# Optimization experiments

Measured on AMD Instinct MI355X. Metric: run time of the kernel, lower is better.

## Reference

```python
import jax, jax.numpy as jnp
import numpy as np

N = 50000   # nodes
IN = 256    # in_feats
OUT = 256   # out_feats
R = 4       # num relations
E = 80000   # edges per relation


def setup_inputs() -> dict:
    key = jax.random.key(0)
    ks = jax.random.split(key, 5)
    x = jax.random.normal(ks[0], (N, IN), jnp.float32)
    src = jax.random.randint(ks[1], (R, E), 0, N, jnp.int32)
    dst = jax.random.randint(ks[2], (R, E), 0, N, jnp.int32)
    # xavier_uniform with relu gain sqrt(2)
    limit = np.sqrt(2.0) * np.sqrt(6.0 / (IN + OUT))
    weight = jax.random.uniform(ks[3], (R, IN, OUT), jnp.float32, -limit, limit)
    self_loop_weight = jax.random.uniform(ks[4], (IN, OUT), jnp.float32, -limit, limit)
    bias = jnp.zeros((OUT,), jnp.float32)
    return dict(x=x, src=src, dst=dst, weight=weight,
                self_loop_weight=self_loop_weight, bias=bias)


def reference(x, src, dst, weight, self_loop_weight, bias):
    n = x.shape[0]

    def per_rel(s, d, W):
        # GraphConv(norm='right', weight=W): sum incoming messages, divide by
        # in-degree (clamped to 1), then matmul (in_feats == out_feats path).
        agg = jax.ops.segment_sum(x[s], d, num_segments=n)            # [N, IN]
        deg = jax.ops.segment_sum(jnp.ones(d.shape, x.dtype), d, num_segments=n)
        agg = agg / jnp.maximum(deg, 1.0)[:, None]
        return agg @ W                                                # [N, OUT]

    # HeteroGraphConv default aggregation: sum over relations
    msg = jax.vmap(per_rel)(src, dst, weight).sum(axis=0)             # [N, OUT]
    out = msg + x @ self_loop_weight + bias
    return jax.nn.relu(out)
```

## Files before the change

### kernel.cpp

```cpp
#include <hip/hip_runtime.h>

#define NODES 50000
#define FEAT  256
#define RELS  4
#define EDGES 80000
#define NEDGE (RELS * EDGES)
#define NB    (RELS * NODES)
#define NBSC  196

typedef __bf16 bf16x8  __attribute__((ext_vector_type(8)));
typedef float  floatx4 __attribute__((ext_vector_type(4)));

struct BF8U { union { unsigned short u[8]; bf16x8 v; uint4 q; }; };

static __device__ __forceinline__ unsigned short f2bf(float f) {
  union { float f; unsigned u; } v; v.f = f;
  unsigned r = v.u + 0x7FFFu + ((v.u >> 16) & 1u);
  return (unsigned short)(r >> 16);
}
static __device__ __forceinline__ bf16x8 cvt8(const float* p, float s) {
  float4 a = ((const float4*)p)[0], b = ((const float4*)p)[1];
  BF8U r;
  r.u[0] = f2bf(a.x * s); r.u[1] = f2bf(a.y * s);
  r.u[2] = f2bf(a.z * s); r.u[3] = f2bf(a.w * s);
  r.u[4] = f2bf(b.x * s); r.u[5] = f2bf(b.y * s);
  r.u[6] = f2bf(b.z * s); r.u[7] = f2bf(b.w * s);
  return r.v;
}

__global__ __launch_bounds__(256) void zero_kernel(unsigned* __restrict__ cnt) {
  int i = blockIdx.x * 256 + threadIdx.x;
  if (i < NB) cnt[i] = 0u;
}

__global__ __launch_bounds__(256) void count_kernel(const int* __restrict__ dst,
                                                    unsigned* __restrict__ cnt) {
  int e = blockIdx.x * 256 + threadIdx.x;
  if (e < NEDGE) atomicAdd(&cnt[(e / EDGES) * NODES + dst[e]], 1u);
}

__global__ __launch_bounds__(256) void scan1_kernel(const unsigned* __restrict__ cnt,
                                                    unsigned* __restrict__ bsum) {
  __shared__ unsigned red[4];
  int t = threadIdx.x;
  int i = blockIdx.x * 1024 + t * 4;
  unsigned s = 0;
  if (i + 3 < NB) {
    uint4 v = *(const uint4*)(cnt + i);
    s = v.x + v.y + v.z + v.w;
  } else {
    for (int j = 0; j < 4; ++j) if (i + j < NB) s += cnt[i + j];
  }
  for (int o = 32; o > 0; o >>= 1) s += __shfl_down(s, o);
  if ((t & 63) == 0) red[t >> 6] = s;
  __syncthreads();
  if (t == 0) bsum[blockIdx.x] = red[0] + red[1] + red[2] + red[3];
}

__global__ __launch_bounds__(256) void scan2_kernel(unsigned* __restrict__ bsum) {
  __shared__ unsigned sa[256], sb[256];
  int t = threadIdx.x;
  unsigned v = (t < NBSC) ? bsum[t] : 0u;
  sa[t] = v;
  __syncthreads();
  unsigned* pin = sa; unsigned* pout = sb;
  for (int d = 1; d < 256; d <<= 1) {
    pout[t] = pin[t] + ((t >= d) ? pin[t - d] : 0u);
    __syncthreads();
    unsigned* tmp = pin; pin = pout; pout = tmp;
  }
  if (t < NBSC) bsum[t] = pin[t] - v;
}

__global__ __launch_bounds__(256) void scan3_kernel(const unsigned* __restrict__ cnt,
                                                    const unsigned* __restrict__ bsum,
                                                    unsigned* __restrict__ off,
                                                    unsigned* __restrict__ cur) {
  __shared__ unsigned sa[256], sb[256];
  int t = threadIdx.x;
  int i = blockIdx.x * 1024 + t * 4;
  uint4 v = {0u, 0u, 0u, 0u};
  if (i + 3 < NB) {
    v = *(const uint4*)(cnt + i);
  } else {
    unsigned tmp[4] = {0u, 0u, 0u, 0u};
    for (int j = 0; j < 4; ++j) if (i + j < NB) tmp[j] = cnt[i + j];
    v.x = tmp[0]; v.y = tmp[1]; v.z = tmp[2]; v.w = tmp[3];
  }
  unsigned s = v.x + v.y + v.z + v.w;
  sa[t] = s;
  __syncthreads();
  unsigned* pin = sa; unsigned* pout = sb;
  for (int d = 1; d < 256; d <<= 1) {
    pout[t] = pin[t] + ((t >= d) ? pin[t - d] : 0u);
    __syncthreads();
    unsigned* tmp = pin; pin = pout; pout = tmp;
  }
  unsigned base = bsum[blockIdx.x] + pin[t] - s;
  uint4 o;
  o.x = base; o.y = o.x + v.x; o.z = o.y + v.y; o.w = o.z + v.z;
  if (i + 3 < NB) {
    *(uint4*)(off + i) = o;
    *(uint4*)(cur + i) = o;
  } else {
    unsigned oo[4] = {o.x, o.y, o.z, o.w};
    for (int j = 0; j < 4; ++j) if (i + j < NB) { off[i + j] = oo[j]; cur[i + j] = oo[j]; }
  }
  if (blockIdx.x == 0 && t == 0) off[NB] = NEDGE;
}

__global__ __launch_bounds__(256) void fill_kernel(const int* __restrict__ src,
                                                   const int* __restrict__ dst,
                                                   unsigned* __restrict__ cur,
                                                   unsigned* __restrict__ epk) {
  int e = blockIdx.x * 256 + threadIdx.x;
  if (e < NEDGE) {
    int r = e / EDGES;
    unsigned pos = atomicAdd(&cur[r * NODES + dst[e]], 1u);
    epk[pos] = (unsigned)src[e];
  }
}

__global__ __launch_bounds__(256) void prepack_kernel(const float* __restrict__ w,
                                                      const float* __restrict__ sw,
                                                      unsigned short* __restrict__ bpk) {
  int t = blockIdx.x * 256 + threadIdx.x;
  int ln = t & 63, nc = (t >> 6) & 15, kc = t >> 10;
  int col = nc * 16 + (ln & 15);
  int row0 = kc * 32 + (ln >> 4) * 8;
  BF8U vv;
#pragma unroll
  for (int j = 0; j < 8; ++j) {
    int gk = row0 + j;
    int c = gk >> 8, kr = gk & 255;
    const float* sp = (c < 4) ? (w + (size_t)c * 65536) : sw;
    vv.u[j] = f2bf(sp[(size_t)kr * 256 + col]);
  }
  ((uint4*)bpk)[t] = vv.q;
}

__global__ __launch_bounds__(256, 3) void fused_kernel(
    const float* __restrict__ x, const unsigned* __restrict__ off,
    const unsigned* __restrict__ epk, const unsigned short* __restrict__ bpk,
    const float* __restrict__ bias, float* __restrict__ out) {
  __shared__ uint4 sA[2048];
  const int tid = threadIdx.x;
  const int lane = tid & 63, wave = tid >> 6;
  const int quad = lane >> 4, l15 = lane & 15;
  const int m0 = blockIdx.x * 64;
  const int nbase = wave * 4;
  const uint4* bp4 = (const uint4*)bpk;
  const bool fast = (m0 + 64 <= NODES);
  uint2* sA2 = (uint2*)sA;
  const int wslot = lane >> 1;

  floatx4 acc[4][4] = {};
  bf16x8 b0[4], b1[4];
  BF8U a0[4], a1[4];

#define LOAD_B(kc, dst)                                                        \
  {                                                                            \
    _Pragma("unroll") for (int ns = 0; ns < 4; ++ns) {                         \
      BF8U t_; t_.q = bp4[(size_t)(kc) * 1024 + (nbase + ns) * 64 + lane];     \
      dst[ns] = t_.v;                                                          \
    }                                                                          \
  }
#define READ_A(k2, dst)                                                        \
  { _Pragma("unroll") for (int ms = 0; ms < 4; ++ms)                           \
      dst[ms].q = sA[(ms * 16 + l15) * 32 + (((k2) * 4 + quad) ^ (l15 & 7))]; }
#define MFMA16(af, bf)                                                         \
  _Pragma("unroll") for (int ms = 0; ms < 4; ++ms)                             \
    _Pragma("unroll") for (int ns = 0; ns < 4; ++ns)                           \
      acc[ms][ns] = __builtin_amdgcn_mfma_f32_16x16x32_bf16(af[ms].v, bf[ns],  \
                                                            acc[ms][ns], 0, 0, 0);
#define STORE_ROW(row, va, sc)                                                 \
  {                                                                            \
    unsigned short o4_[4] = { f2bf((va).x * (sc)), f2bf((va).y * (sc)),        \
                              f2bf((va).z * (sc)), f2bf((va).w * (sc)) };      \
    sA2[((row) * 32 + (wslot ^ ((row) & 7))) * 2 + (lane & 1)] =               \
        *(const uint2*)o4_;                                                    \
  }

  for (int c = 0; c < 5; ++c) {
    __syncthreads();
    LOAD_B(c * 8, b0);
    if (c < 4) {
      if (fast) {
        unsigned bbase = (unsigned)c * NODES + (unsigned)(m0 + wave * 16);
        unsigned ov = (lane < 17) ? off[bbase + (unsigned)lane] : 0u;
        unsigned lo_w = (unsigned)__shfl((int)ov, 0);
        unsigned hi_w = (unsigned)__shfl((int)ov, 16);
        unsigned eidx = lo_w + (unsigned)lane;
        int ev = (eidx < hi_w) ? (int)epk[eidx] : 0;
        for (int i = 0; i < 16; ++i) {
          int row = wave * 16 + i;
          unsigned lo = (unsigned)__shfl((int)ov, i);
          unsigned hi = (unsigned)__shfl((int)ov, i + 1);
          float4 va = {0.f, 0.f, 0.f, 0.f};
          unsigned e = lo;
          for (; e + 2 <= hi; e += 2) {
            unsigned r0 = e - lo_w, r1 = e + 1u - lo_w;
            int s0 = (r0 < 64u) ? __shfl(ev, (int)r0) : (int)epk[e];
            int s1 = (r1 < 64u) ? __shfl(ev, (int)r1) : (int)epk[e + 1];
            float4 v0 = *(const float4*)(x + (size_t)s0 * FEAT + lane * 4);
            float4 v1 = *(const float4*)(x + (size_t)s1 * FEAT + lane * 4);
            va.x += v0.x + v1.x; va.y += v0.y + v1.y;
            va.z += v0.z + v1.z; va.w += v0.w + v1.w;
          }
          if (e < hi) {
            unsigned r0 = e - lo_w;
            int s = (r0 < 64u) ? __shfl(ev, (int)r0) : (int)epk[e];
            float4 v = *(const float4*)(x + (size_t)s * FEAT + lane * 4);
            va.x += v.x; va.y += v.y; va.z += v.z; va.w += v.w;
          }
          unsigned dg = hi - lo;
          float sc = 1.0f / (float)(dg ? dg : 1u);
          STORE_ROW(row, va, sc);
        }
      } else {
        for (int i = 0; i < 16; ++i) {
          int row = wave * 16 + i;
          int g = m0 + row; if (g >= NODES) g = NODES - 1;
          unsigned b = (unsigned)c * NODES + (unsigned)g;
          unsigned lo = off[b], hi = off[b + 1];
          float4 va = {0.f, 0.f, 0.f, 0.f};
          unsigned e = lo;
          for (; e + 2 <= hi; e += 2) {
            int s0 = (int)epk[e], s1 = (int)epk[e + 1];
            float4 v0 = *(const float4*)(x + (size_t)s0 * FEAT + lane * 4);
            float4 v1 = *(const float4*)(x + (size_t)s1 * FEAT + lane * 4);
            va.x += v0.x + v1.x; va.y += v0.y + v1.y;
            va.z += v0.z + v1.z; va.w += v0.w + v1.w;
          }
          if (e < hi) {
            int s = (int)epk[e];
            float4 v = *(const float4*)(x + (size_t)s * FEAT + lane * 4);
            va.x += v.x; va.y += v.y; va.z += v.z; va.w += v.w;
          }
          unsigned dg = hi - lo;
          float sc = 1.0f / (float)(dg ? dg : 1u);
          STORE_ROW(row, va, sc);
        }
      }
    } else {
      for (int i = 0; i < 16; ++i) {
        int row = wave * 16 + i;
        int g = m0 + row; if (g >= NODES) g = NODES - 1;
        float4 va = *(const float4*)(x + (size_t)g * FEAT + lane * 4);
        STORE_ROW(row, va, 1.0f);
      }
    }
    __syncthreads();
    READ_A(0, a0);
#pragma unroll
    for (int k2 = 0; k2 < 8; k2 += 2) {
      LOAD_B(c * 8 + k2 + 1, b1);
      READ_A(k2 + 1, a1);
      MFMA16(a0, b0);
      if (k2 + 2 < 8) { LOAD_B(c * 8 + k2 + 2, b0); READ_A(k2 + 2, a0); }
      MFMA16(a1, b1);
    }
  }
#undef LOAD_B
#undef READ_A
#undef MFMA16
#undef STORE_ROW

#pragma unroll
  for (int ms = 0; ms < 4; ++ms)
#pragma unroll
    for (int i = 0; i < 4; ++i) {
      int row = m0 + ms * 16 + quad * 4 + i;
      if (row < NODES) {
        float* op = out + (size_t)row * FEAT + wave * 64;
#pragma unroll
        for (int ns = 0; ns < 4; ++ns) {
          int col = ns * 16 + l15;
          op[col] = fmaxf(acc[ms][ns][i] + bias[wave * 64 + col], 0.0f);
        }
      }
    }
}

#define AROWS 128
#define ASTR  260
#define ABLK  512

__global__ __launch_bounds__(ABLK) void rgcn_fallback(
    const float* __restrict__ x, const int* __restrict__ src,
    const int* __restrict__ dst, const float* __restrict__ w,
    const float* __restrict__ sw, const float* __restrict__ bias,
    float* __restrict__ out) {
  __shared__ float sAgg[AROWS * ASTR];
  __shared__ unsigned short sB[8192];
  __shared__ unsigned sDeg[AROWS];
  const int tid = threadIdx.x, wave = tid >> 6, lane = tid & 63;
  const int quad = lane >> 4, l15 = lane & 15;
  const int m0 = blockIdx.x * AROWS;
  const int wrow = wave * 16;
  floatx4 acc[16] = {};
  const floatx4 fz = {0.f, 0.f, 0.f, 0.f};
  for (int r = 0; r < RELS; ++r) {
    for (int t = tid; t < (AROWS * ASTR) / 4; t += ABLK) ((floatx4*)sAgg)[t] = fz;
    if (tid < AROWS) sDeg[tid] = 0u;
    __syncthreads();
    const int4* sr4 = (const int4*)(src + r * EDGES);
    const int4* dr4 = (const int4*)(dst + r * EDGES);
    for (int i0 = tid; i0 < 20480; i0 += ABLK) {
      int4 d4 = {-1, -1, -1, -1}, s4 = {0, 0, 0, 0};
      if (i0 < EDGES / 4) { d4 = dr4[i0]; s4 = sr4[i0]; }
      int dd[4] = {d4.x, d4.y, d4.z, d4.w};
      int ss[4] = {s4.x, s4.y, s4.z, s4.w};
#pragma unroll
      for (int j = 0; j < 4; ++j) {
        unsigned u = (unsigned)(dd[j] - m0);
        unsigned long long mb = __ballot(u < (unsigned)AROWS);
        while (mb) {
          int jl = (int)__ffsll(mb) - 1; mb &= mb - 1;
          int s = __shfl(ss[j], jl);
          int ul = __shfl((int)u, jl);
          if (lane == 0) atomicAdd(&sDeg[ul], 1u);
          const float* xp = x + (size_t)s * FEAT + lane;
          float* ap = sAgg + ul * ASTR + lane;
#pragma unroll
          for (int k = 0; k < 4; ++k) atomicAdd(ap + k * 64, xp[k * 64]);
        }
      }
    }
    __syncthreads();
    unsigned dg = sDeg[wrow + l15];
    float rs = 1.0f / (float)(dg ? dg : 1u);
    const float* Wc = w + (size_t)r * 65536;
    for (int kc = 0; kc < 8; ++kc) {
      for (int t = tid; t < 1024; t += ABLK) {
        int ln = t & 63, nc = t >> 6;
        const float* wp = Wc + (size_t)(kc * 32 + (ln >> 4) * 8) * 256 + nc * 16 + (ln & 15);
        BF8U vv;
#pragma unroll
        for (int j = 0; j < 8; ++j) vv.u[j] = f2bf(wp[(size_t)j * 256]);
        ((uint4*)sB)[t] = vv.q;
      }
      __syncthreads();
      bf16x8 a = cvt8(&sAgg[(wrow + l15) * ASTR + kc * 32 + quad * 8], rs);
#pragma unroll
      for (int ns = 0; ns < 16; ++ns) {
        BF8U b8; b8.q = ((const uint4*)sB)[ns * 64 + lane];
        acc[ns] = __builtin_amdgcn_mfma_f32_16x16x32_bf16(a, b8.v, acc[ns], 0, 0, 0);
      }
      __syncthreads();
    }
  }
  {
    int row = m0 + wrow + l15;
    if (row >= NODES) row = NODES - 1;
    for (int kc = 0; kc < 8; ++kc) {
      for (int t = tid; t < 1024; t += ABLK) {
        int ln = t & 63, nc = t >> 6;
        const float* wp = sw + (size_t)(kc * 32 + (ln >> 4) * 8) * 256 + nc * 16 + (ln & 15);
        BF8U vv;
#pragma unroll
        for (int j = 0; j < 8; ++j) vv.u[j] = f2bf(wp[(size_t)j * 256]);
        ((uint4*)sB)[t] = vv.q;
      }
      __syncthreads();
      bf16x8 a = cvt8(x + (size_t)row * FEAT + kc * 32 + quad * 8, 1.0f);
#pragma unroll
      for (int ns = 0; ns < 16; ++ns) {
        BF8U b8; b8.q = ((const uint4*)sB)[ns * 64 + lane];
        acc[ns] = __builtin_amdgcn_mfma_f32_16x16x32_bf16(a, b8.v, acc[ns], 0, 0, 0);
      }
      __syncthreads();
    }
  }
#pragma unroll
  for (int i = 0; i < 4; ++i) {
    int row = m0 + wrow + quad * 4 + i;
    if (row < NODES) {
      float* op = out + (size_t)row * FEAT;
#pragma unroll
      for (int ns = 0; ns < 16; ++ns) {
        int col = ns * 16 + l15;
        op[col] = fmaxf(acc[ns][i] + bias[col], 0.0f);
      }
    }
  }
}

extern "C" void kernel_launch(void* const* d_in, const int* in_sizes, int n_in,
                              void* d_out, int out_size, void* d_ws, size_t ws_size,
                              hipStream_t stream) {
  const float* x    = (const float*)d_in[0];
  const int*   src  = (const int*)d_in[1];
  const int*   dst  = (const int*)d_in[2];
  const float* w    = (const float*)d_in[3];
  const float* sw   = (const float*)d_in[4];
  const float* bias = (const float*)d_in[5];
  float*       out  = (float*)d_out;
  char* ws = (char*)d_ws;

  const size_t NEED = 4336400;
  if (ws_size >= NEED) {
    unsigned short* bpk = (unsigned short*)ws;
    unsigned* cnt  = (unsigned*)(ws + 655360);
    unsigned* off  = (unsigned*)(ws + 1455360);
    unsigned* cur  = (unsigned*)(ws + 2255376);
    unsigned* epk  = (unsigned*)(ws + 3055376);
    unsigned* bsum = (unsigned*)(ws + 4335376);

    zero_kernel<<<(NB + 255) / 256, 256, 0, stream>>>(cnt);
    count_kernel<<<(NEDGE + 255) / 256, 256, 0, stream>>>(dst, cnt);
    scan1_kernel<<<NBSC, 256, 0, stream>>>(cnt, bsum);
    scan2_kernel<<<1, 256, 0, stream>>>(bsum);
    scan3_kernel<<<NBSC, 256, 0, stream>>>(cnt, bsum, off, cur);
    fill_kernel<<<(NEDGE + 255) / 256, 256, 0, stream>>>(src, dst, cur, epk);
    prepack_kernel<<<160, 256, 0, stream>>>(w, sw, bpk);
    fused_kernel<<<(NODES + 63) / 64, 256, 0, stream>>>(x, off, epk, bpk, bias, out);
  } else {
    rgcn_fallback<<<391, ABLK, 0, stream>>>(x, src, dst, w, sw, bias, out);
  }
}
```

Measured before the change: 282.7 us.

## Halve fused tile rows and interleave four-row gathers for more memory parallelism

Shrinks the fused block tile from 64 to 32 nodes, which doubles the grid, halves the LDS footprint and accumulators, and raises the occupancy hint to 4. The gather loop now walks four destination rows at once so that more independent x-row loads are in flight per wave, and the self-loop rows are loaded in a batch before being stored. The first B tile load moves after the gather phase. In exchange, each B fragment is reused across fewer rows, so weight traffic from L2 per node doubles. The interleaved loop also adds divergent-style predication when the four rows have different degrees.

```diff
diff --git a/kernel.cpp b/kernel.cpp
--- a/kernel.cpp
+++ b/kernel.cpp
@@ -139,24 +139,24 @@
   ((uint4*)bpk)[t] = vv.q;
 }
 
-__global__ __launch_bounds__(256, 3) void fused_kernel(
+__global__ __launch_bounds__(256, 4) void fused_kernel(
     const float* __restrict__ x, const unsigned* __restrict__ off,
     const unsigned* __restrict__ epk, const unsigned short* __restrict__ bpk,
     const float* __restrict__ bias, float* __restrict__ out) {
-  __shared__ uint4 sA[2048];
+  __shared__ uint4 sA[1024];
   const int tid = threadIdx.x;
   const int lane = tid & 63, wave = tid >> 6;
   const int quad = lane >> 4, l15 = lane & 15;
-  const int m0 = blockIdx.x * 64;
+  const int m0 = blockIdx.x * 32;
   const int nbase = wave * 4;
   const uint4* bp4 = (const uint4*)bpk;
-  const bool fast = (m0 + 64 <= NODES);
+  const bool fast = (m0 + 32 <= NODES);
   uint2* sA2 = (uint2*)sA;
   const int wslot = lane >> 1;
 
-  floatx4 acc[4][4] = {};
+  floatx4 acc[2][4] = {};
   bf16x8 b0[4], b1[4];
-  BF8U a0[4], a1[4];
+  BF8U a0[2], a1[2];
 
 #define LOAD_B(kc, dst)                                                        \
   {                                                                            \
@@ -166,10 +166,10 @@
     }                                                                          \
   }
 #define READ_A(k2, dst)                                                        \
-  { _Pragma("unroll") for (int ms = 0; ms < 4; ++ms)                           \
+  { _Pragma("unroll") for (int ms = 0; ms < 2; ++ms)                           \
       dst[ms].q = sA[(ms * 16 + l15) * 32 + (((k2) * 4 + quad) ^ (l15 & 7))]; }
-#define MFMA16(af, bf)                                                         \
-  _Pragma("unroll") for (int ms = 0; ms < 4; ++ms)                             \
+#define MFMA8(af, bf)                                                          \
+  _Pragma("unroll") for (int ms = 0; ms < 2; ++ms)                             \
     _Pragma("unroll") for (int ns = 0; ns < 4; ++ns)                           \
       acc[ms][ns] = __builtin_amdgcn_mfma_f32_16x16x32_bf16(af[ms].v, bf[ns],  \
                                                             acc[ms][ns], 0, 0, 0);
@@ -183,56 +183,72 @@
 
   for (int c = 0; c < 5; ++c) {
     __syncthreads();
-    LOAD_B(c * 8, b0);
     if (c < 4) {
       if (fast) {
-        unsigned bbase = (unsigned)c * NODES + (unsigned)(m0 + wave * 16);
-        unsigned ov = (lane < 17) ? off[bbase + (unsigned)lane] : 0u;
+        unsigned bbase = (unsigned)c * NODES + (unsigned)(m0 + wave * 8);
+        unsigned ov = (lane < 9) ? off[bbase + (unsigned)lane] : 0u;
         unsigned lo_w = (unsigned)__shfl((int)ov, 0);
-        unsigned hi_w = (unsigned)__shfl((int)ov, 16);
-        unsigned eidx = lo_w + (unsigned)lane;
-        int ev = (eidx < hi_w) ? (int)epk[eidx] : 0;
-        for (int i = 0; i < 16; ++i) {
-          int row = wave * 16 + i;
-          unsigned lo = (unsigned)__shfl((int)ov, i);
-          unsigned hi = (unsigned)__shfl((int)ov, i + 1);
-          float4 va = {0.f, 0.f, 0.f, 0.f};
-          unsigned e = lo;
-          for (; e + 2 <= hi; e += 2) {
-            unsigned r0 = e - lo_w, r1 = e + 1u - lo_w;
-            int s0 = (r0 < 64u) ? __shfl(ev, (int)r0) : (int)epk[e];
-            int s1 = (r1 < 64u) ? __shfl(ev, (int)r1) : (int)epk[e + 1];
-            float4 v0 = *(const float4*)(x + (size_t)s0 * FEAT + lane * 4);
-            float4 v1 = *(const float4*)(x + (size_t)s1 * FEAT + lane * 4);
-            va.x += v0.x + v1.x; va.y += v0.y + v1.y;
-            va.z += v0.z + v1.z; va.w += v0.w + v1.w;
+        unsigned hi_w = (unsigned)__shfl((int)ov, 8);
+        unsigned cnt = hi_w - lo_w;
+        int ev = ((unsigned)lane < cnt) ? (int)epk[lo_w + (unsigned)lane] : 0;
+#pragma unroll
+        for (int i4 = 0; i4 < 8; i4 += 4) {
+          unsigned lo0 = (unsigned)__shfl((int)ov, i4 + 0);
+          unsigned lo1 = (unsigned)__shfl((int)ov, i4 + 1);
+          unsigned lo2 = (unsigned)__shfl((int)ov, i4 + 2);
+          unsigned lo3 = (unsigned)__shfl((int)ov, i4 + 3);
+          unsigned hi3 = (unsigned)__shfl((int)ov, i4 + 4);
+          unsigned e0 = lo0, e1 = lo1, e2 = lo2, e3 = lo3;
+          unsigned h0 = lo1, h1 = lo2, h2 = lo3, h3 = hi3;
+          float4 va0 = {0.f,0.f,0.f,0.f}, va1 = va0, va2 = va0, va3 = va0;
+          while ((e0 < h0) | (e1 < h1) | (e2 < h2) | (e3 < h3)) {
+            bool c0 = e0 < h0, c1 = e1 < h1, c2 = e2 < h2, c3 = e3 < h3;
+            float4 v0, v1, v2, v3;
+            if (c0) {
+              unsigned rl = e0 - lo_w;
+              int s = (rl < 64u) ? __shfl(ev, (int)rl) : (int)epk[e0];
+              v0 = *(const float4*)(x + (size_t)s * FEAT + lane * 4);
+            }
+            if (c1) {
+              unsigned rl = e1 - lo_w;
+              int s = (rl < 64u) ? __shfl(ev, (int)rl) : (int)epk[e1];
+              v1 = *(const float4*)(x + (size_t)s * FEAT + lane * 4);
+            }
+            if (c2) {
+              unsigned rl = e2 - lo_w;
+              int s = (rl < 64u) ? __shfl(ev, (int)rl) : (int)epk[e2];
+              v2 = *(const float4*)(x + (size_t)s * FEAT + lane * 4);
+            }
+            if (c3) {
+              unsigned rl = e3 - lo_w;
+              int s = (rl < 64u) ? __shfl(ev, (int)rl) : (int)epk[e3];
+              v3 = *(const float4*)(x + (size_t)s * FEAT + lane * 4);
+            }
+            if (c0) { va0.x += v0.x; va0.y += v0.y; va0.z += v0.z; va0.w += v0.w; ++e0; }
+            if (c1) { va1.x += v1.x; va1.y += v1.y; va1.z += v1.z; va1.w += v1.w; ++e1; }
+            if (c2) { va2.x += v2.x; va2.y += v2.y; va2.z += v2.z; va2.w += v2.w; ++e2; }
+            if (c3) { va3.x += v3.x; va3.y += v3.y; va3.z += v3.z; va3.w += v3.w; ++e3; }
           }
-          if (e < hi) {
-            unsigned r0 = e - lo_w;
-            int s = (r0 < 64u) ? __shfl(ev, (int)r0) : (int)epk[e];
-            float4 v = *(const float4*)(x + (size_t)s * FEAT + lane * 4);
-            va.x += v.x; va.y += v.y; va.z += v.z; va.w += v.w;
+          {
+            unsigned d0 = h0 - lo0, d1 = h1 - lo1, d2 = h2 - lo2, d3 = h3 - lo3;
+            float s0 = 1.0f / (float)(d0 ? d0 : 1u);
+            float s1 = 1.0f / (float)(d1 ? d1 : 1u);
+            float s2 = 1.0f / (float)(d2 ? d2 : 1u);
+            float s3 = 1.0f / (float)(d3 ? d3 : 1u);
+            STORE_ROW(wave * 8 + i4 + 0, va0, s0);
+            STORE_ROW(wave * 8 + i4 + 1, va1, s1);
+            STORE_ROW(wave * 8 + i4 + 2, va2, s2);
+            STORE_ROW(wave * 8 + i4 + 3, va3, s3);
           }
-          unsigned dg = hi - lo;
-          float sc = 1.0f / (float)(dg ? dg : 1u);
-          STORE_ROW(row, va, sc);
         }
       } else {
-        for (int i = 0; i < 16; ++i) {
-          int row = wave * 16 + i;
+        for (int i = 0; i < 8; ++i) {
+          int row = wave * 8 + i;
           int g = m0 + row; if (g >= NODES) g = NODES - 1;
           unsigned b = (unsigned)c * NODES + (unsigned)g;
           unsigned lo = off[b], hi = off[b + 1];
           float4 va = {0.f, 0.f, 0.f, 0.f};
-          unsigned e = lo;
-          for (; e + 2 <= hi; e += 2) {
-            int s0 = (int)epk[e], s1 = (int)epk[e + 1];
-            float4 v0 = *(const float4*)(x + (size_t)s0 * FEAT + lane * 4);
-            float4 v1 = *(const float4*)(x + (size_t)s1 * FEAT + lane * 4);
-            va.x += v0.x + v1.x; va.y += v0.y + v1.y;
-            va.z += v0.z + v1.z; va.w += v0.w + v1.w;
-          }
-          if (e < hi) {
+          for (unsigned e = lo; e < hi; ++e) {
             int s = (int)epk[e];
             float4 v = *(const float4*)(x + (size_t)s * FEAT + lane * 4);
             va.x += v.x; va.y += v.y; va.z += v.z; va.w += v.w;
@@ -243,31 +259,34 @@
         }
       }
     } else {
-      for (int i = 0; i < 16; ++i) {
-        int row = wave * 16 + i;
-        int g = m0 + row; if (g >= NODES) g = NODES - 1;
-        float4 va = *(const float4*)(x + (size_t)g * FEAT + lane * 4);
-        STORE_ROW(row, va, 1.0f);
-      }
-    }
+      float4 vs[8];
+#pragma unroll
+      for (int i = 0; i < 8; ++i) {
+        int g = m0 + wave * 8 + i; if (g >= NODES) g = NODES - 1;
+        vs[i] = *(const float4*)(x + (size_t)g * FEAT + lane * 4);
+      }
+#pragma unroll
+      for (int i = 0; i < 8; ++i) STORE_ROW(wave * 8 + i, vs[i], 1.0f);
+    }
+    LOAD_B(c * 8, b0);
     __syncthreads();
     READ_A(0, a0);
 #pragma unroll
     for (int k2 = 0; k2 < 8; k2 += 2) {
       LOAD_B(c * 8 + k2 + 1, b1);
       READ_A(k2 + 1, a1);
-      MFMA16(a0, b0);
+      MFMA8(a0, b0);
       if (k2 + 2 < 8) { LOAD_B(c * 8 + k2 + 2, b0); READ_A(k2 + 2, a0); }
-      MFMA16(a1, b1);
+      MFMA8(a1, b1);
     }
   }
 #undef LOAD_B
 #undef READ_A
-#undef MFMA16
+#undef MFMA8
 #undef STORE_ROW
 
 #pragma unroll
-  for (int ms = 0; ms < 4; ++ms)
+  for (int ms = 0; ms < 2; ++ms)
 #pragma unroll
     for (int i = 0; i < 4; ++i) {
       int row = m0 + ms * 16 + quad * 4 + i;
@@ -414,7 +433,7 @@
     scan3_kernel<<<NBSC, 256, 0, stream>>>(cnt, bsum, off, cur);
     fill_kernel<<<(NEDGE + 255) / 256, 256, 0, stream>>>(src, dst, cur, epk);
     prepack_kernel<<<160, 256, 0, stream>>>(w, sw, bpk);
-    fused_kernel<<<(NODES + 63) / 64, 256, 0, stream>>>(x, off, epk, bpk, bias, out);
+    fused_kernel<<<(NODES + 31) / 32, 256, 0, stream>>>(x, off, epk, bpk, bias, out);
   } else {
     rgcn_fallback<<<391, ABLK, 0, stream>>>(x, src, dst, w, sw, bias, out);
   }
```

After: 293.3 us. 3.8% more time.
